# Optimization experiments

Hardware: AMD Instinct MI355X
Metric: run time of the kernel (lower is better)

## Reference

```python
import jax, jax.numpy as jnp
import numpy as np

B, SEQ_LEN, PRED_LEN, LABEL_LEN, PERIOD, N_CH = 32, 2048, 1024, 512, 256, 256
K = SEQ_LEN // PERIOD   # seg_num_x = 8
L = PRED_LEN // PERIOD  # seg_num_y = 4
EPS = 1e-5


def setup_inputs() -> dict:
    key = jax.random.key(0)
    k1, k2, k3, k4, k5, k6, k7 = jax.random.split(key, 7)
    x_enc = jax.random.normal(k1, (B, SEQ_LEN, N_CH), jnp.float32)
    x_mark_enc = jax.random.normal(k2, (B, SEQ_LEN, 4), jnp.float32)
    x_dec = jax.random.normal(k3, (B, LABEL_LEN + PRED_LEN, N_CH), jnp.float32)
    x_mark_dec = jax.random.normal(k4, (B, LABEL_LEN + PRED_LEN, 4), jnp.float32)
    # base_model abstracted as a linear map on the time axis of a [B, PERIOD, N] segment.
    # Scaled ~1/sqrt(P) so repeated powers (up to K+L-1 = 11) stay numerically tame.
    W_base = jax.random.normal(k5, (PERIOD, PERIOD), jnp.float32) * (0.9 / np.sqrt(PERIOD))
    # new_encoders[j]: nn.Linear(seg_num_x, 1) -> weight row [K] + bias scalar per j.
    W_enc = jax.random.normal(k6, (L, K), jnp.float32) * (1.0 / np.sqrt(K))
    b_enc = jax.random.normal(k7, (L,), jnp.float32) * 0.01
    return {"x_enc": x_enc, "x_mark_enc": x_mark_enc, "x_dec": x_dec,
            "x_mark_dec": x_mark_dec, "W_base": W_base, "W_enc": W_enc, "b_enc": b_enc}


def reference(x_enc, x_mark_enc, x_dec, x_mark_dec, W_base, W_enc, b_enc):
    Bv, S, N = x_enc.shape
    # per-series normalization over time (means is .detach()'d in torch; fwd math identical)
    means = jnp.mean(x_enc, axis=1, keepdims=True)                  # [B,1,N]
    xc = x_enc - means
    stdev = jnp.sqrt(jnp.var(xc, axis=1, keepdims=True) + EPS)      # [B,1,N]
    xn = xc / stdev

    # split into K segments of length PERIOD: [K, B, P, N]
    segs = xn.reshape(Bv, K, PERIOD, N).transpose(1, 0, 2, 3)

    # x_res[l][k] = base_model applied (K - k + l) times to segment k.
    # base(x) = einsum('qp,bpn->bqn', W_base, x), so m applications = W_base^m.
    def step(c, _):
        nxt = W_base @ c
        return nxt, nxt
    _, rest = jax.lax.scan(step, W_base, None, length=K + L - 2)
    powers = jnp.concatenate([W_base[None], rest], axis=0)          # powers[i] = W^(i+1)

    exps = (K - jnp.arange(K))[None, :] + jnp.arange(L)[:, None]    # [L,K]
    Wlk = powers[exps - 1]                                          # [L,K,P,P]
    x_res = jnp.einsum('lkqp,kbpn->lkbqn', Wlk, segs)               # [L,K,B,P,N]

    # dec_out_part[l] = sum_k W_enc[l,k] * x_res[l][k] + b_enc[l] * ones
    dec = jnp.einsum('lk,lkbqn->lbqn', W_enc, x_res) + b_enc[:, None, None, None]
    dec = dec.transpose(1, 0, 2, 3).reshape(Bv, L * PERIOD, N)      # cat over time

    # de-normalize
    dec = dec * stdev[:, 0, :][:, None, :] + means[:, 0, :][:, None, :]
    return dec[:, -PRED_LEN:, :]
```

## Files before the change

### kernel.cpp

```cpp
#include <hip/hip_runtime.h>
#include <cstdint>
#include <cstddef>


typedef unsigned short ushort_t;
typedef unsigned int uint_t;
typedef __attribute__((ext_vector_type(8))) short bf16x8;
typedef __attribute__((ext_vector_type(16))) float f32x16;

__device__ __forceinline__ ushort_t f32_to_bf16(float f) {
    uint_t u = __float_as_uint(f);
    u += 0x7FFFu + ((u >> 16) & 1u);
    return (ushort_t)(u >> 16);
}
__device__ __forceinline__ float bf16_to_f32(ushort_t h) {
    return __uint_as_float((uint_t)h << 16);
}

struct PowOps { int sa[4]; int sb[4]; int sd[4]; };

__global__ void powmul(const float* __restrict__ Wb, float* __restrict__ Pw, PowOps ops) {
    __shared__ float As[4 * 256];
    const int mat = blockIdx.x;
    const int r0  = blockIdx.y * 4;
    const int tid = threadIdx.x;
    const float* A  = (ops.sa[mat] < 0) ? Wb : Pw + (size_t)ops.sa[mat] * 65536;
    const float* Bm = (ops.sb[mat] < 0) ? Wb : Pw + (size_t)ops.sb[mat] * 65536;
    float* C        = Pw + (size_t)ops.sd[mat] * 65536;
#pragma unroll
    for (int i = 0; i < 4; ++i) As[i * 256 + tid] = A[(size_t)(r0 + i) * 256 + tid];
    __syncthreads();
    float a0 = 0.f, a1 = 0.f, a2 = 0.f, a3 = 0.f;
    for (int p = 0; p < 256; p += 8) {
        float bv[8];
#pragma unroll
        for (int u = 0; u < 8; ++u) bv[u] = Bm[(size_t)(p + u) * 256 + tid];
#pragma unroll
        for (int u = 0; u < 8; ++u) {
            a0 += As[0 * 256 + p + u] * bv[u];
            a1 += As[1 * 256 + p + u] * bv[u];
            a2 += As[2 * 256 + p + u] * bv[u];
            a3 += As[3 * 256 + p + u] * bv[u];
        }
    }
    C[(size_t)(r0 + 0) * 256 + tid] = a0;
    C[(size_t)(r0 + 1) * 256 + tid] = a1;
    C[(size_t)(r0 + 2) * 256 + tid] = a2;
    C[(size_t)(r0 + 3) * 256 + tid] = a3;
}

__global__ void prep(const float* __restrict__ x, ushort_t* __restrict__ Xt,
                     float* __restrict__ ps1, float* __restrict__ ps2,
                     const float* __restrict__ Pw, const float* __restrict__ Wb,
                     ushort_t* __restrict__ Pb, float* __restrict__ prs) {
    __shared__ float lds[64 * 65];
    __shared__ float red1[16 * 64];
    __shared__ float red2[16 * 64];
    const int bid = blockIdx.x;
    const int tid = threadIdx.x;
    if (bid < 4096) {
        const int st = bid & 31;
        const int nt = (bid >> 5) & 3;
        const int b  = bid >> 7;
        const int c = tid & 15, r = tid >> 4;
        const int s0 = st * 64;
        float s1[4] = {0,0,0,0}, s2[4] = {0,0,0,0};
#pragma unroll
        for (int it = 0; it < 4; ++it) {
            const int ii = r + it * 16;
            const float4 v = *(const float4*)(x + ((size_t)b * 2048 + s0 + ii) * 256 + nt * 64 + c * 4);
            const float vv[4] = {v.x, v.y, v.z, v.w};
#pragma unroll
            for (int jj = 0; jj < 4; ++jj) {
                lds[ii * 65 + c * 4 + jj] = vv[jj];
                s1[jj] += vv[jj]; s2[jj] += vv[jj] * vv[jj];
            }
        }
#pragma unroll
        for (int jj = 0; jj < 4; ++jj) { red1[r * 64 + c * 4 + jj] = s1[jj]; red2[r * 64 + c * 4 + jj] = s2[jj]; }
        __syncthreads();
        if (tid < 64) {
            float a = 0.f, q = 0.f;
#pragma unroll
            for (int rr = 0; rr < 16; ++rr) { a += red1[rr * 64 + tid]; q += red2[rr * 64 + tid]; }
            const size_t o = (size_t)st * 8192 + b * 256 + nt * 64 + tid;
            ps1[o] = a; ps2[o] = q;
        }
#pragma unroll
        for (int step = 0; step < 8; ++step) {
            const int npr = step * 8 + (tid >> 5);
            const int sp  = (tid & 31) * 2;
            const float f0 = lds[sp * 65 + npr];
            const float f1 = lds[(sp + 1) * 65 + npr];
            const uint_t packed = (uint_t)f32_to_bf16(f0) | ((uint_t)f32_to_bf16(f1) << 16);
            *(uint_t*)(Xt + ((size_t)b * 256 + nt * 64 + npr) * 2048 + s0 + sp) = packed;
        }
    } else {
        const int ib = bid - 4096;
        const int e  = ib >> 2;
        const int rq = ib & 3;
        const int q  = rq * 64 + (tid >> 2);
        const int cc = tid & 3;
        uint2* dst = (uint2*)(Pb + (size_t)e * 65536 + q * 256 + cc * 64);
        float s = 0.f;
        if (e == 0) {
#pragma unroll
            for (int i = 0; i < 16; ++i) {
                uint2 o; o.x = 0u; o.y = 0u;
                const int col0 = cc * 64 + i * 4;
                if (q >= col0 && q < col0 + 4) {
                    const int j = q - col0;
                    if (j == 0) o.x = 0x3F80u; else if (j == 1) o.x = 0x3F800000u;
                    else if (j == 2) o.y = 0x3F80u; else o.y = 0x3F800000u;
                }
                dst[i] = o;
            }
            s = 1.0f;
        } else {
            const float* src = (e == 1) ? Wb : (Pw + (size_t)(e - 2) * 65536);
            const float4* sp = (const float4*)(src + (size_t)q * 256 + cc * 64);
#pragma unroll
            for (int i = 0; i < 16; ++i) {
                const float4 v = sp[i];
                const ushort_t h0 = f32_to_bf16(v.x), h1 = f32_to_bf16(v.y);
                const ushort_t h2 = f32_to_bf16(v.z), h3 = f32_to_bf16(v.w);
                s += bf16_to_f32(h0) + bf16_to_f32(h1) + bf16_to_f32(h2) + bf16_to_f32(h3);
                uint2 o; o.x = (uint_t)h0 | ((uint_t)h1 << 16); o.y = (uint_t)h2 | ((uint_t)h3 << 16);
                dst[i] = o;
            }
        }
        s += __shfl_xor(s, 1);
        s += __shfl_xor(s, 2);
        if (cc == 0) prs[e * 256 + q] = s;
    }
}

#define GLOAD_LDS16(gsrc, ldst) \
    __builtin_amdgcn_global_load_lds((const __attribute__((address_space(1))) void*)(gsrc), \
                                     (__attribute__((address_space(3))) void*)(ldst), 16, 0, 0)

__global__ __launch_bounds__(256, 2) void gemm_v(
    const ushort_t* __restrict__ Pb,
    const ushort_t* __restrict__ Xt,
    ushort_t* __restrict__ vt,
    const float* __restrict__ ps1, const float* __restrict__ ps2,
    const float* __restrict__ prs, const float* __restrict__ Wenc,
    float* __restrict__ meanv, float* __restrict__ stdv, float* __restrict__ rsA)
{
    __shared__ ushort_t sAa[3][4096];
    __shared__ ushort_t sBb[3][8192];

    const int bid = blockIdx.x;
    const int tid = threadIdx.x;
    if (bid >= 512) {
        const int idx = bid - 512;
        if (idx < 32) {
            const int b = idx;
            float s = 0.f, q = 0.f;
#pragma unroll
            for (int st = 0; st < 32; ++st) {
                s += ps1[(size_t)st * 8192 + b * 256 + tid];
                q += ps2[(size_t)st * 8192 + b * 256 + tid];
            }
            const float mean = s * (1.0f / 2048.0f);
            float var = q * (1.0f / 2048.0f) - mean * mean;
            var = fmaxf(var, 0.0f);
            meanv[b * 256 + tid] = mean;
            stdv [b * 256 + tid] = sqrtf(var + 1e-5f);
        } else {
            const int l = idx - 32;
            float u = 0.f;
#pragma unroll
            for (int k = 0; k < 8; ++k) u += Wenc[l * 8 + k] * prs[(8 - k) * 256 + tid];
            float* uf = (float*)&sAa[0][0];
            uf[tid] = u;
            __syncthreads();
            const uint2* rp = (const uint2*)(Pb + (size_t)l * 65536 + tid * 256);
            float s = 0.f;
#pragma unroll
            for (int i = 0; i < 64; ++i) {
                const uint2 v = rp[i];
                s += bf16_to_f32((ushort_t)(v.x & 0xffff)) * uf[i * 4 + 0]
                   + bf16_to_f32((ushort_t)(v.x >> 16))    * uf[i * 4 + 1]
                   + bf16_to_f32((ushort_t)(v.y & 0xffff)) * uf[i * 4 + 2]
                   + bf16_to_f32((ushort_t)(v.y >> 16))    * uf[i * 4 + 3];
            }
            rsA[l * 256 + tid] = s;
        }
        return;
    }

    const int xcd  = bid & 7;
    const int g    = bid >> 3;
    const int colT = xcd + ((g & 7) << 3);
    const int k    = g >> 3;
    const int e    = 8 - k;

    const int lane = tid & 63;
    const int w    = tid >> 6;
    const int wm   = w >> 1, wn = w & 1;
    const int li   = lane & 31, lg = lane >> 5;
    const int lq3  = (li >> 1) & 3;
    const int lrow = 2 * (lane >> 3) + ((lane >> 2) & 1);
    const int kc   = (lane & 3) ^ ((lane >> 3) & 3);

    const ushort_t* xtb = Xt + (size_t)(colT * 128) * 2048 + k * 256;
    const ushort_t* pbb = Pb + (size_t)e * 65536;

#define VSTAGE(bf_, kt_) do { \
    const int p0_ = (kt_) * 32 + kc * 8; \
    GLOAD_LDS16(xtb + (size_t)(w * 32 + 0  + lrow) * 2048 + p0_, &sAa[bf_][(w * 32 + 0)  * 32]); \
    GLOAD_LDS16(xtb + (size_t)(w * 32 + 16 + lrow) * 2048 + p0_, &sAa[bf_][(w * 32 + 16) * 32]); \
    GLOAD_LDS16(pbb + (w * 64 + 0  + lrow) * 256 + p0_, &sBb[bf_][(w * 64 + 0)  * 32]); \
    GLOAD_LDS16(pbb + (w * 64 + 16 + lrow) * 256 + p0_, &sBb[bf_][(w * 64 + 16) * 32]); \
    GLOAD_LDS16(pbb + (w * 64 + 32 + lrow) * 256 + p0_, &sBb[bf_][(w * 64 + 32) * 32]); \
    GLOAD_LDS16(pbb + (w * 64 + 48 + lrow) * 256 + p0_, &sBb[bf_][(w * 64 + 48) * 32]); \
} while (0)

    f32x16 acc[2][4];
#pragma unroll
    for (int mm = 0; mm < 2; ++mm)
#pragma unroll
        for (int nn = 0; nn < 4; ++nn)
#pragma unroll
            for (int rr = 0; rr < 16; ++rr) acc[mm][nn][rr] = 0.0f;

    VSTAGE(0, 0);
    VSTAGE(1, 1);

#define VKT(kt_) do { \
    if ((kt_) < 7) { asm volatile("s_waitcnt vmcnt(6)" ::: "memory"); } \
    else           { asm volatile("s_waitcnt vmcnt(0)" ::: "memory"); } \
    __builtin_amdgcn_s_barrier(); \
    asm volatile("" ::: "memory"); \
    const ushort_t* pa_ = &sAa[(kt_) % 3][0]; \
    const ushort_t* px_ = &sBb[(kt_) % 3][0]; \
    bf16x8 af[2][2], xf[2][4]; \
    _Pragma("unroll") \
    for (int ks = 0; ks < 2; ++ks) { \
        const int sl = ((ks << 1) + lg) ^ lq3; \
        const int ro = (li >> 1) * 64 + (li & 1) * 32 + sl * 8; \
        af[ks][0] = *(const bf16x8*)(pa_ + wm * 2048 + ro); \
        af[ks][1] = *(const bf16x8*)(pa_ + wm * 2048 + 1024 + ro); \
        xf[ks][0] = *(const bf16x8*)(px_ + wn * 4096 + ro); \
        xf[ks][1] = *(const bf16x8*)(px_ + wn * 4096 + 1024 + ro); \
        xf[ks][2] = *(const bf16x8*)(px_ + wn * 4096 + 2048 + ro); \
        xf[ks][3] = *(const bf16x8*)(px_ + wn * 4096 + 3072 + ro); \
    } \
    if ((kt_) < 6) { VSTAGE(((kt_) + 2) % 3, (kt_) + 2); } \
    __builtin_amdgcn_s_setprio(1); \
    _Pragma("unroll") \
    for (int ks = 0; ks < 2; ++ks) \
        _Pragma("unroll") \
        for (int mm = 0; mm < 2; ++mm) \
            _Pragma("unroll") \
            for (int nn = 0; nn < 4; ++nn) \
                acc[mm][nn] = __builtin_amdgcn_mfma_f32_32x32x16_bf16(af[ks][mm], xf[ks][nn], acc[mm][nn], 0, 0, 0); \
    __builtin_amdgcn_s_setprio(0); \
    asm volatile("" ::: "memory"); \
} while (0)

    VKT(0); VKT(1); VKT(2); VKT(3); VKT(4); VKT(5); VKT(6); VKT(7);
#undef VKT
#undef VSTAGE

    ushort_t* vb = vt + (size_t)k * 2097152;
#pragma unroll
    for (int mm = 0; mm < 2; ++mm)
#pragma unroll
        for (int nn = 0; nn < 4; ++nn) {
            const int q = wn * 128 + nn * 32 + li;
#pragma unroll
            for (int rr = 0; rr < 16; ++rr) {
                const int c = colT * 128 + wm * 64 + mm * 32 + ((rr & 3) + 8 * (rr >> 2) + 4 * lg);
                vb[(size_t)c * 256 + q] = f32_to_bf16(acc[mm][nn][rr]);
            }
        }
}

__global__ void combine(const ushort_t* __restrict__ vt, const float* __restrict__ Wenc,
                        ushort_t* __restrict__ c) {
    const int t   = threadIdx.x;
    const int col = blockIdx.x * 8 + (t >> 5);
    const size_t off = (size_t)col * 256 + (t & 31) * 8;
    float a0[8] = {0,0,0,0,0,0,0,0}, a1[8] = {0,0,0,0,0,0,0,0};
    float a2[8] = {0,0,0,0,0,0,0,0}, a3[8] = {0,0,0,0,0,0,0,0};
#pragma unroll
    for (int k = 0; k < 8; ++k) {
        const bf16x8 v = *(const bf16x8*)(vt + (size_t)k * 2097152 + off);
        const float w0 = Wenc[0 * 8 + k], w1 = Wenc[1 * 8 + k];
        const float w2 = Wenc[2 * 8 + k], w3 = Wenc[3 * 8 + k];
#pragma unroll
        for (int j = 0; j < 8; ++j) {
            const float f = bf16_to_f32((ushort_t)v[j]);
            a0[j] += w0 * f; a1[j] += w1 * f; a2[j] += w2 * f; a3[j] += w3 * f;
        }
    }
    bf16x8 o0, o1, o2, o3;
#pragma unroll
    for (int j = 0; j < 8; ++j) {
        o0[j] = (short)f32_to_bf16(a0[j]); o1[j] = (short)f32_to_bf16(a1[j]);
        o2[j] = (short)f32_to_bf16(a2[j]); o3[j] = (short)f32_to_bf16(a3[j]);
    }
    *(bf16x8*)(c + 0 * 2097152 + off) = o0;
    *(bf16x8*)(c + 1 * 2097152 + off) = o1;
    *(bf16x8*)(c + 2 * 2097152 + off) = o2;
    *(bf16x8*)(c + 3 * 2097152 + off) = o3;
}

__global__ __launch_bounds__(256, 2) void gemm2(
    const ushort_t* __restrict__ Pb, const ushort_t* __restrict__ c,
    const float* __restrict__ meanv, const float* __restrict__ stdv,
    const float* __restrict__ rsA, const float* __restrict__ benc,
    float* __restrict__ out)
{
    __shared__ ushort_t sAa[3][4096];
    __shared__ ushort_t sBb[3][4096];

    const int bid  = blockIdx.x;
    const int xcd  = bid & 7;
    const int g    = bid >> 3;
    const int colT = xcd + ((g & 7) << 3);
    const int rest = g >> 3;
    const int l    = rest >> 1;
    const int qpT  = rest & 1;

    const int tid  = threadIdx.x;
    const int lane = tid & 63;
    const int w    = tid >> 6;
    const int wm   = w >> 1, wn = w & 1;
    const int li   = lane & 31, lg = lane >> 5;
    const int lq3  = (li >> 1) & 3;
    const int lrow = 2 * (lane >> 3) + ((lane >> 2) & 1);
    const int kc   = (lane & 3) ^ ((lane >> 3) & 3);

    const ushort_t* ab = Pb + (size_t)l * 65536 + (size_t)(qpT * 128) * 256;
    const ushort_t* cb = c + ((size_t)l * 8192 + colT * 128) * 256;

#define GSTAGE(bf_, kt_) do { \
    const int p0_ = (kt_) * 32 + kc * 8; \
// ... 56 lines not shown
        mn[nn] = meanv[col];
        sd[nn] = stdv [col];
    }
#pragma unroll
    for (int mm = 0; mm < 2; ++mm)
#pragma unroll
        for (int nn = 0; nn < 2; ++nn) {
            const int col = colT * 128 + wn * 64 + nn * 32 + li;
            const int bq = col >> 8, nq = col & 255;
            const float ben = be * sd[nn];
#pragma unroll
            for (int rr = 0; rr < 16; ++rr) {
                const int trow = l * 256 + qpT * 128 + wm * 64 + mm * 32
                               + ((rr & 3) + 8 * (rr >> 2) + 4 * lg);
                out[((size_t)bq * 1024 + trow) * 256 + nq] =
                    acc[mm][nn][rr] + mn[nn] * (1.0f - rsA[trow]) + ben;
            }
        }
}

extern "C" void kernel_launch(void* const* d_in, const int* in_sizes, int n_in,
                              void* d_out, int out_size, void* d_ws, size_t ws_size,
                              hipStream_t stream) {
    (void)in_sizes; (void)n_in; (void)out_size; (void)ws_size;
    const float* x_enc  = (const float*)d_in[0];
    const float* W_base = (const float*)d_in[4];
    const float* W_enc  = (const float*)d_in[5];
    const float* b_enc  = (const float*)d_in[6];
    float* out = (float*)d_out;

    char* ws = (char*)d_ws;
    float*    wsP    = (float*)(ws);
    ushort_t* wsPb   = (ushort_t*)(ws + 0x200000);
    float*    wsPrs  = (float*)(ws + 0x320000);
    float*    wsS1   = (float*)(ws + 0x330000);
    float*    wsS2   = (float*)(ws + 0x430000);
    float*    wsMean = (float*)(ws + 0x530000);
    float*    wsStd  = (float*)(ws + 0x540000);
    float*    wsRsA  = (float*)(ws + 0x550000);
    ushort_t* wsXt   = (ushort_t*)(ws + 0x600000);
    ushort_t* wsC    = (ushort_t*)(ws + 0x600000);
    ushort_t* wsVt   = (ushort_t*)(ws + 0x2600000);

    { PowOps o{{-1, 0, 0, 0}, {-1, 0, 0, 0}, {0, 0, 0, 0}};
      powmul<<<dim3(1, 64), 256, 0, stream>>>(W_base, wsP, o); }
    { PowOps o{{0, 0, 0, 0}, {-1, 0, 0, 0}, {1, 2, 0, 0}};
      powmul<<<dim3(2, 64), 256, 0, stream>>>(W_base, wsP, o); }
    { PowOps o{{2, 2, 2, 2}, {-1, 0, 1, 2}, {3, 4, 5, 6}};
      powmul<<<dim3(4, 64), 256, 0, stream>>>(W_base, wsP, o); }

    prep<<<4132, 256, 0, stream>>>(x_enc, wsXt, wsS1, wsS2, wsP, W_base, wsPb, wsPrs);

    gemm_v<<<548, 256, 0, stream>>>(wsPb, wsXt, wsVt, wsS1, wsS2, wsPrs, W_enc,
                                    wsMean, wsStd, wsRsA);

    combine<<<1024, 256, 0, stream>>>(wsVt, W_enc, wsC);

    gemm2<<<512, 256, 0, stream>>>(wsPb, wsC, wsMean, wsStd, wsRsA, b_enc, out);
}
```

Before: 98.77 us.

## Fuse input transpose, bf16 conversion and statistics into the first GEMM

The separate prep pass that transposed x_enc into a bf16 buffer and computed partial sums is removed. gemm_v now loads fp32 x tiles directly, accumulates sum and sum-of-squares in registers, and builds swizzled bf16 MFMA fragments in LDS through a scratch buffer. The mean/std and row-sum side work moves into the combine kernel. This drops a full write and read of the transposed activation tensor, but it adds LDS traffic, extra barriers and register pressure inside the GEMM main loop.

New measurement: 126.0 us. +27.6%, slower.

```diff
diff --git a/kernel.cpp b/kernel.cpp
--- a/kernel.cpp
+++ b/kernel.cpp
@@ -49,90 +49,45 @@
     C[(size_t)(r0 + 3) * 256 + tid] = a3;
 }
 
-__global__ void prep(const float* __restrict__ x, ushort_t* __restrict__ Xt,
-                     float* __restrict__ ps1, float* __restrict__ ps2,
-                     const float* __restrict__ Pw, const float* __restrict__ Wb,
-                     ushort_t* __restrict__ Pb, float* __restrict__ prs) {
-    __shared__ float lds[64 * 65];
-    __shared__ float red1[16 * 64];
-    __shared__ float red2[16 * 64];
-    const int bid = blockIdx.x;
+__global__ void prepPb(const float* __restrict__ Pw, const float* __restrict__ Wb,
+                       ushort_t* __restrict__ Pb, float* __restrict__ prs) {
+    const int ib = blockIdx.x;
+    const int e  = ib >> 2;
+    const int rq = ib & 3;
     const int tid = threadIdx.x;
-    if (bid < 4096) {
-        const int st = bid & 31;
-        const int nt = (bid >> 5) & 3;
-        const int b  = bid >> 7;
-        const int c = tid & 15, r = tid >> 4;
-        const int s0 = st * 64;
-        float s1[4] = {0,0,0,0}, s2[4] = {0,0,0,0};
-#pragma unroll
-        for (int it = 0; it < 4; ++it) {
-            const int ii = r + it * 16;
-            const float4 v = *(const float4*)(x + ((size_t)b * 2048 + s0 + ii) * 256 + nt * 64 + c * 4);
-            const float vv[4] = {v.x, v.y, v.z, v.w};
-#pragma unroll
-            for (int jj = 0; jj < 4; ++jj) {
-                lds[ii * 65 + c * 4 + jj] = vv[jj];
-                s1[jj] += vv[jj]; s2[jj] += vv[jj] * vv[jj];
+    const int q  = rq * 64 + (tid >> 2);
+    const int cc = tid & 3;
+    uint2* dst = (uint2*)(Pb + (size_t)e * 65536 + q * 256 + cc * 64);
+    float s = 0.f;
+    if (e == 0) {
+#pragma unroll
+        for (int i = 0; i < 16; ++i) {
+            uint2 o; o.x = 0u; o.y = 0u;
+            const int col0 = cc * 64 + i * 4;
+            if (q >= col0 && q < col0 + 4) {
+                const int j = q - col0;
+                if (j == 0) o.x = 0x3F80u; else if (j == 1) o.x = 0x3F800000u;
+                else if (j == 2) o.y = 0x3F80u; else o.y = 0x3F800000u;
             }
-        }
-#pragma unroll
-        for (int jj = 0; jj < 4; ++jj) { red1[r * 64 + c * 4 + jj] = s1[jj]; red2[r * 64 + c * 4 + jj] = s2[jj]; }
-        __syncthreads();
-        if (tid < 64) {
-            float a = 0.f, q = 0.f;
-#pragma unroll
-            for (int rr = 0; rr < 16; ++rr) { a += red1[rr * 64 + tid]; q += red2[rr * 64 + tid]; }
-            const size_t o = (size_t)st * 8192 + b * 256 + nt * 64 + tid;
-            ps1[o] = a; ps2[o] = q;
-        }
-#pragma unroll
-        for (int step = 0; step < 8; ++step) {
-            const int npr = step * 8 + (tid >> 5);
-            const int sp  = (tid & 31) * 2;
-            const float f0 = lds[sp * 65 + npr];
-            const float f1 = lds[(sp + 1) * 65 + npr];
-            const uint_t packed = (uint_t)f32_to_bf16(f0) | ((uint_t)f32_to_bf16(f1) << 16);
-            *(uint_t*)(Xt + ((size_t)b * 256 + nt * 64 + npr) * 2048 + s0 + sp) = packed;
-        }
+            dst[i] = o;
+        }
+        s = 1.0f;
     } else {
-        const int ib = bid - 4096;
-        const int e  = ib >> 2;
-        const int rq = ib & 3;
-        const int q  = rq * 64 + (tid >> 2);
-        const int cc = tid & 3;
-        uint2* dst = (uint2*)(Pb + (size_t)e * 65536 + q * 256 + cc * 64);
-        float s = 0.f;
-        if (e == 0) {
-#pragma unroll
-            for (int i = 0; i < 16; ++i) {
-                uint2 o; o.x = 0u; o.y = 0u;
-                const int col0 = cc * 64 + i * 4;
-                if (q >= col0 && q < col0 + 4) {
-                    const int j = q - col0;
-                    if (j == 0) o.x = 0x3F80u; else if (j == 1) o.x = 0x3F800000u;
-                    else if (j == 2) o.y = 0x3F80u; else o.y = 0x3F800000u;
-                }
-                dst[i] = o;
-            }
-            s = 1.0f;
-        } else {
-            const float* src = (e == 1) ? Wb : (Pw + (size_t)(e - 2) * 65536);
-            const float4* sp = (const float4*)(src + (size_t)q * 256 + cc * 64);
-#pragma unroll
-            for (int i = 0; i < 16; ++i) {
-                const float4 v = sp[i];
-                const ushort_t h0 = f32_to_bf16(v.x), h1 = f32_to_bf16(v.y);
-                const ushort_t h2 = f32_to_bf16(v.z), h3 = f32_to_bf16(v.w);
-                s += bf16_to_f32(h0) + bf16_to_f32(h1) + bf16_to_f32(h2) + bf16_to_f32(h3);
-                uint2 o; o.x = (uint_t)h0 | ((uint_t)h1 << 16); o.y = (uint_t)h2 | ((uint_t)h3 << 16);
-                dst[i] = o;
-            }
-        }
-        s += __shfl_xor(s, 1);
-        s += __shfl_xor(s, 2);
-        if (cc == 0) prs[e * 256 + q] = s;
-    }
+        const float* src = (e == 1) ? Wb : (Pw + (size_t)(e - 2) * 65536);
+        const float4* sp = (const float4*)(src + (size_t)q * 256 + cc * 64);
+#pragma unroll
+        for (int i = 0; i < 16; ++i) {
+            const float4 v = sp[i];
+            const ushort_t h0 = f32_to_bf16(v.x), h1 = f32_to_bf16(v.y);
+            const ushort_t h2 = f32_to_bf16(v.z), h3 = f32_to_bf16(v.w);
+            s += bf16_to_f32(h0) + bf16_to_f32(h1) + bf16_to_f32(h2) + bf16_to_f32(h3);
+            uint2 o; o.x = (uint_t)h0 | ((uint_t)h1 << 16); o.y = (uint_t)h2 | ((uint_t)h3 << 16);
+            dst[i] = o;
+        }
+    }
+    s += __shfl_xor(s, 1);
+    s += __shfl_xor(s, 2);
+    if (cc == 0) prs[e * 256 + q] = s;
 }
 
 #define GLOAD_LDS16(gsrc, ldst) \
@@ -140,62 +95,20 @@
                                      (__attribute__((address_space(3))) void*)(ldst), 16, 0, 0)
 
 __global__ __launch_bounds__(256, 2) void gemm_v(
-    const ushort_t* __restrict__ Pb,
-    const ushort_t* __restrict__ Xt,
+    const ushort_t* __restrict__ Pb, const float* __restrict__ x,
     ushort_t* __restrict__ vt,
-    const float* __restrict__ ps1, const float* __restrict__ ps2,
-    const float* __restrict__ prs, const float* __restrict__ Wenc,
-    float* __restrict__ meanv, float* __restrict__ stdv, float* __restrict__ rsA)
+    float* __restrict__ psS1, float* __restrict__ psS2)
 {
-    __shared__ ushort_t sAa[3][4096];
-    __shared__ ushort_t sBb[3][8192];
-
-    const int bid = blockIdx.x;
-    const int tid = threadIdx.x;
-    if (bid >= 512) {
-        const int idx = bid - 512;
-        if (idx < 32) {
-            const int b = idx;
-            float s = 0.f, q = 0.f;
-#pragma unroll
-            for (int st = 0; st < 32; ++st) {
-                s += ps1[(size_t)st * 8192 + b * 256 + tid];
-                q += ps2[(size_t)st * 8192 + b * 256 + tid];
-            }
-            const float mean = s * (1.0f / 2048.0f);
-            float var = q * (1.0f / 2048.0f) - mean * mean;
-            var = fmaxf(var, 0.0f);
-            meanv[b * 256 + tid] = mean;
-            stdv [b * 256 + tid] = sqrtf(var + 1e-5f);
-        } else {
-            const int l = idx - 32;
-            float u = 0.f;
-#pragma unroll
-            for (int k = 0; k < 8; ++k) u += Wenc[l * 8 + k] * prs[(8 - k) * 256 + tid];
-            float* uf = (float*)&sAa[0][0];
-            uf[tid] = u;
-            __syncthreads();
-            const uint2* rp = (const uint2*)(Pb + (size_t)l * 65536 + tid * 256);
-            float s = 0.f;
-#pragma unroll
-            for (int i = 0; i < 64; ++i) {
-                const uint2 v = rp[i];
-                s += bf16_to_f32((ushort_t)(v.x & 0xffff)) * uf[i * 4 + 0]
-                   + bf16_to_f32((ushort_t)(v.x >> 16))    * uf[i * 4 + 1]
-                   + bf16_to_f32((ushort_t)(v.y & 0xffff)) * uf[i * 4 + 2]
-                   + bf16_to_f32((ushort_t)(v.y >> 16))    * uf[i * 4 + 3];
-            }
-            rsA[l * 256 + tid] = s;
-        }
-        return;
-    }
-
-    const int xcd  = bid & 7;
-    const int g    = bid >> 3;
-    const int colT = xcd + ((g & 7) << 3);
-    const int k    = g >> 3;
+    __shared__ ushort_t sA[2][4096];
+    __shared__ ushort_t sB[3][8192];
+    __shared__ float    scr[32 * 128];
+
+    const int bid  = blockIdx.x;
+    const int k    = bid & 7;
+    const int colT = bid >> 3;
     const int e    = 8 - k;
 
+    const int tid  = threadIdx.x;
     const int lane = tid & 63;
     const int w    = tid >> 6;
     const int wm   = w >> 1, wn = w & 1;
@@ -204,17 +117,58 @@
     const int lrow = 2 * (lane >> 3) + ((lane >> 2) & 1);
     const int kc   = (lane & 3) ^ ((lane >> 3) & 3);
 
-    const ushort_t* xtb = Xt + (size_t)(colT * 128) * 2048 + k * 256;
     const ushort_t* pbb = Pb + (size_t)e * 65536;
-
-#define VSTAGE(bf_, kt_) do { \
+    const int b  = colT >> 1;
+    const int n0 = (colT & 1) * 128;
+    const float* xseg = x + ((size_t)b * 2048 + k * 256) * 256 + n0;
+
+    const int xp = tid >> 5;
+    const int xn = (tid & 31) * 4;
+
+    float4 xr[4];
+    float s1[4] = {0, 0, 0, 0}, s2[4] = {0, 0, 0, 0};
+
+#define BSTAGE(bf_, kt_) do { \
     const int p0_ = (kt_) * 32 + kc * 8; \
-    GLOAD_LDS16(xtb + (size_t)(w * 32 + 0  + lrow) * 2048 + p0_, &sAa[bf_][(w * 32 + 0)  * 32]); \
-    GLOAD_LDS16(xtb + (size_t)(w * 32 + 16 + lrow) * 2048 + p0_, &sAa[bf_][(w * 32 + 16) * 32]); \
-    GLOAD_LDS16(pbb + (w * 64 + 0  + lrow) * 256 + p0_, &sBb[bf_][(w * 64 + 0)  * 32]); \
-    GLOAD_LDS16(pbb + (w * 64 + 16 + lrow) * 256 + p0_, &sBb[bf_][(w * 64 + 16) * 32]); \
-    GLOAD_LDS16(pbb + (w * 64 + 32 + lrow) * 256 + p0_, &sBb[bf_][(w * 64 + 32) * 32]); \
-    GLOAD_LDS16(pbb + (w * 64 + 48 + lrow) * 256 + p0_, &sBb[bf_][(w * 64 + 48) * 32]); \
+    GLOAD_LDS16(pbb + (w * 64 + 0  + lrow) * 256 + p0_, &sB[bf_][(w * 64 + 0)  * 32]); \
+    GLOAD_LDS16(pbb + (w * 64 + 16 + lrow) * 256 + p0_, &sB[bf_][(w * 64 + 16) * 32]); \
+    GLOAD_LDS16(pbb + (w * 64 + 32 + lrow) * 256 + p0_, &sB[bf_][(w * 64 + 32) * 32]); \
+    GLOAD_LDS16(pbb + (w * 64 + 48 + lrow) * 256 + p0_, &sB[bf_][(w * 64 + 48) * 32]); \
+} while (0)
+
+#define XLOAD(kt_) do { \
+    _Pragma("unroll") \
+    for (int i_ = 0; i_ < 4; ++i_) \
+        xr[i_] = *(const float4*)(xseg + (size_t)((kt_) * 32 + xp + 8 * i_) * 256 + xn); \
+} while (0)
+
+#define SCRW() do { \
+    _Pragma("unroll") \
+    for (int i_ = 0; i_ < 4; ++i_) { \
+        *(float4*)(scr + (xp + 8 * i_) * 128 + xn) = xr[i_]; \
+        s1[0] += xr[i_].x; s2[0] += xr[i_].x * xr[i_].x; \
+        s1[1] += xr[i_].y; s2[1] += xr[i_].y * xr[i_].y; \
+        s1[2] += xr[i_].z; s2[2] += xr[i_].z * xr[i_].z; \
+        s1[3] += xr[i_].w; s2[3] += xr[i_].w * xr[i_].w; \
+    } \
+} while (0)
+
+#define FRAGBUILD(buf_) do { \
+    const int R_ = tid >> 1; \
+    const int swz_ = (R_ >> 1) & 3; \
+    _Pragma("unroll") \
+    for (int cc_ = 0; cc_ < 2; ++cc_) { \
+        const int pc_ = (tid & 1) * 2 + cc_; \
+        uint_t pk_[4]; \
+        _Pragma("unroll") \
+        for (int u_ = 0; u_ < 4; ++u_) { \
+            const float v0_ = scr[(pc_ * 8 + 2 * u_ + 0) * 128 + R_]; \
+            const float v1_ = scr[(pc_ * 8 + 2 * u_ + 1) * 128 + R_]; \
+            pk_[u_] = (uint_t)f32_to_bf16(v0_) | ((uint_t)f32_to_bf16(v1_) << 16); \
+        } \
+        uint4 o_; o_.x = pk_[0]; o_.y = pk_[1]; o_.z = pk_[2]; o_.w = pk_[3]; \
+        *(uint4*)((char*)&sA[buf_][0] + R_ * 64 + ((pc_ ^ swz_) << 4)) = o_; \
+    } \
 } while (0)
 
     f32x16 acc[2][4];
@@ -225,16 +179,26 @@
 #pragma unroll
             for (int rr = 0; rr < 16; ++rr) acc[mm][nn][rr] = 0.0f;
 
-    VSTAGE(0, 0);
-    VSTAGE(1, 1);
+    XLOAD(0);
+    SCRW();
+    asm volatile("s_waitcnt lgkmcnt(0)" ::: "memory");
+    __builtin_amdgcn_s_barrier();
+    asm volatile("" ::: "memory");
+    FRAGBUILD(0);
+    BSTAGE(0, 0);
+    asm volatile("" ::: "memory");
+    XLOAD(1);
+    asm volatile("" ::: "memory");
+    BSTAGE(1, 1);
+    asm volatile("s_waitcnt lgkmcnt(0)" ::: "memory");
 
 #define VKT(kt_) do { \
-    if ((kt_) < 7) { asm volatile("s_waitcnt vmcnt(6)" ::: "memory"); } \
+    if ((kt_) < 7) { asm volatile("s_waitcnt vmcnt(4)" ::: "memory"); } \
     else           { asm volatile("s_waitcnt vmcnt(0)" ::: "memory"); } \
     __builtin_amdgcn_s_barrier(); \
     asm volatile("" ::: "memory"); \
-    const ushort_t* pa_ = &sAa[(kt_) % 3][0]; \
-    const ushort_t* px_ = &sBb[(kt_) % 3][0]; \
+    const ushort_t* pa_ = &sA[(kt_) & 1][0]; \
+    const ushort_t* px_ = &sB[(kt_) % 3][0]; \
     bf16x8 af[2][2], xf[2][4]; \
     _Pragma("unroll") \
     for (int ks = 0; ks < 2; ++ks) { \
@@ -247,7 +211,12 @@
         xf[ks][2] = *(const bf16x8*)(px_ + wn * 4096 + 2048 + ro); \
         xf[ks][3] = *(const bf16x8*)(px_ + wn * 4096 + 3072 + ro); \
     } \
-    if ((kt_) < 6) { VSTAGE(((kt_) + 2) % 3, (kt_) + 2); } \
+    if ((kt_) < 7) { SCRW(); }    \
+    if ((kt_) < 6) { \
+        XLOAD((kt_) + 2); \
+        asm volatile("" ::: "memory"); \
+        BSTAGE(((kt_) + 2) % 3, (kt_) + 2); \
+    } \
     __builtin_amdgcn_s_setprio(1); \
     _Pragma("unroll") \
     for (int ks = 0; ks < 2; ++ks) \
@@ -258,11 +227,21 @@
                 acc[mm][nn] = __builtin_amdgcn_mfma_f32_32x32x16_bf16(af[ks][mm], xf[ks][nn], acc[mm][nn], 0, 0, 0); \
     __builtin_amdgcn_s_setprio(0); \
     asm volatile("" ::: "memory"); \
+    if ((kt_) < 7) { \
+        asm volatile("s_waitcnt lgkmcnt(0)" ::: "memory"); \
+        __builtin_amdgcn_s_barrier(); \
+        asm volatile("" ::: "memory"); \
+        FRAGBUILD(((kt_) + 1) & 1); \
+        asm volatile("s_waitcnt lgkmcnt(0)" ::: "memory"); \
+    } \
 } while (0)
 
     VKT(0); VKT(1); VKT(2); VKT(3); VKT(4); VKT(5); VKT(6); VKT(7);
 #undef VKT
-#undef VSTAGE
+#undef FRAGBUILD
+#undef SCRW
+#undef XLOAD
+#undef BSTAGE
 
     ushort_t* vb = vt + (size_t)k * 2097152;
 #pragma unroll
@@ -276,36 +255,96 @@
                 vb[(size_t)c * 256 + q] = f32_to_bf16(acc[mm][nn][rr]);
             }
         }
+
+    __syncthreads();
+#pragma unroll
+    for (int j = 0; j < 4; ++j) {
+        scr[xp * 128 + xn + j]        = s1[j];
+        scr[1024 + xp * 128 + xn + j] = s2[j];
+    }
+    __syncthreads();
+    if (tid < 128) {
+        float a = 0.f;
+#pragma unroll
+        for (int r = 0; r < 8; ++r) a += scr[r * 128 + tid];
+        psS1[(size_t)k * 8192 + colT * 128 + tid] = a;
+    } else {
+        const int tt = tid - 128;
+        float a = 0.f;
+#pragma unroll
+        for (int r = 0; r < 8; ++r) a += scr[1024 + r * 128 + tt];
+        psS2[(size_t)k * 8192 + colT * 128 + tt] = a;
+    }
 }
 
 __global__ void combine(const ushort_t* __restrict__ vt, const float* __restrict__ Wenc,
-                        ushort_t* __restrict__ c) {
+                        ushort_t* __restrict__ c,
+                        const float* __restrict__ psS1, const float* __restrict__ psS2,
+                        const float* __restrict__ prs, const ushort_t* __restrict__ Pb,
+                        float* __restrict__ meanv, float* __restrict__ stdv,
+                        float* __restrict__ rsA) {
+    __shared__ float uf[256];
+    const int bid = blockIdx.x;
     const int t   = threadIdx.x;
-    const int col = blockIdx.x * 8 + (t >> 5);
-    const size_t off = (size_t)col * 256 + (t & 31) * 8;
-    float a0[8] = {0,0,0,0,0,0,0,0}, a1[8] = {0,0,0,0,0,0,0,0};
-    float a2[8] = {0,0,0,0,0,0,0,0}, a3[8] = {0,0,0,0,0,0,0,0};
-#pragma unroll
-    for (int k = 0; k < 8; ++k) {
-        const bf16x8 v = *(const bf16x8*)(vt + (size_t)k * 2097152 + off);
-        const float w0 = Wenc[0 * 8 + k], w1 = Wenc[1 * 8 + k];
-        const float w2 = Wenc[2 * 8 + k], w3 = Wenc[3 * 8 + k];
+    if (bid < 1024) {
+        const int col = bid * 8 + (t >> 5);
+        const size_t off = (size_t)col * 256 + (t & 31) * 8;
+        float a0[8] = {0,0,0,0,0,0,0,0}, a1[8] = {0,0,0,0,0,0,0,0};
+        float a2[8] = {0,0,0,0,0,0,0,0}, a3[8] = {0,0,0,0,0,0,0,0};
+#pragma unroll
+        for (int k = 0; k < 8; ++k) {
+            const bf16x8 v = *(const bf16x8*)(vt + (size_t)k * 2097152 + off);
+            const float w0 = Wenc[0 * 8 + k], w1 = Wenc[1 * 8 + k];
+            const float w2 = Wenc[2 * 8 + k], w3 = Wenc[3 * 8 + k];
+#pragma unroll
+            for (int j = 0; j < 8; ++j) {
+                const float f = bf16_to_f32((ushort_t)v[j]);
+                a0[j] += w0 * f; a1[j] += w1 * f; a2[j] += w2 * f; a3[j] += w3 * f;
+            }
+        }
+        bf16x8 o0, o1, o2, o3;
 #pragma unroll
         for (int j = 0; j < 8; ++j) {
-            const float f = bf16_to_f32((ushort_t)v[j]);
-            a0[j] += w0 * f; a1[j] += w1 * f; a2[j] += w2 * f; a3[j] += w3 * f;
-        }
-    }
-    bf16x8 o0, o1, o2, o3;
-#pragma unroll
-    for (int j = 0; j < 8; ++j) {
-        o0[j] = (short)f32_to_bf16(a0[j]); o1[j] = (short)f32_to_bf16(a1[j]);
-        o2[j] = (short)f32_to_bf16(a2[j]); o3[j] = (short)f32_to_bf16(a3[j]);
-    }
-    *(bf16x8*)(c + 0 * 2097152 + off) = o0;
-    *(bf16x8*)(c + 1 * 2097152 + off) = o1;
-    *(bf16x8*)(c + 2 * 2097152 + off) = o2;
-    *(bf16x8*)(c + 3 * 2097152 + off) = o3;
+            o0[j] = (short)f32_to_bf16(a0[j]); o1[j] = (short)f32_to_bf16(a1[j]);
+            o2[j] = (short)f32_to_bf16(a2[j]); o3[j] = (short)f32_to_bf16(a3[j]);
+        }
+        *(bf16x8*)(c + 0 * 2097152 + off) = o0;
+        *(bf16x8*)(c + 1 * 2097152 + off) = o1;
+        *(bf16x8*)(c + 2 * 2097152 + off) = o2;
+        *(bf16x8*)(c + 3 * 2097152 + off) = o3;
+    } else if (bid < 1056) {
+        const int b = bid - 1024;
+        const int col = b * 256 + t;
+        float s = 0.f, q = 0.f;
+#pragma unroll
+        for (int k = 0; k < 8; ++k) {
+            s += psS1[(size_t)k * 8192 + col];
+            q += psS2[(size_t)k * 8192 + col];
+        }
+        const float mean = s * (1.0f / 2048.0f);
+        float var = q * (1.0f / 2048.0f) - mean * mean;
+        var = fmaxf(var, 0.0f);
+        meanv[col] = mean;
+        stdv [col] = sqrtf(var + 1e-5f);
+    } else {
+        const int l = bid - 1056;
+        float u = 0.f;
+#pragma unroll
+        for (int k = 0; k < 8; ++k) u += Wenc[l * 8 + k] * prs[(8 - k) * 256 + t];
+        uf[t] = u;
+        __syncthreads();
+        const uint2* rp = (const uint2*)(Pb + (size_t)l * 65536 + t * 256);
+        float s = 0.f;
+#pragma unroll
+        for (int i = 0; i < 64; ++i) {
+            const uint2 v = rp[i];
+            s += bf16_to_f32((ushort_t)(v.x & 0xffff)) * uf[i * 4 + 0]
+               + bf16_to_f32((ushort_t)(v.x >> 16))    * uf[i * 4 + 1]
+               + bf16_to_f32((ushort_t)(v.y & 0xffff)) * uf[i * 4 + 2]
+               + bf16_to_f32((ushort_t)(v.y >> 16))    * uf[i * 4 + 3];
+        }
+        rsA[l * 256 + t] = s;
+    }
 }
 
 __global__ __launch_bounds__(256, 2) void gemm2(
@@ -428,15 +467,14 @@
     char* ws = (char*)d_ws;
     float*    wsP    = (float*)(ws);
     ushort_t* wsPb   = (ushort_t*)(ws + 0x200000);
-    float*    wsPrs  = (float*)(ws + 0x320000);
-    float*    wsS1   = (float*)(ws + 0x330000);
-    float*    wsS2   = (float*)(ws + 0x430000);
-    float*    wsMean = (float*)(ws + 0x530000);
-    float*    wsStd  = (float*)(ws + 0x540000);
-    float*    wsRsA  = (float*)(ws + 0x550000);
-    ushort_t* wsXt   = (ushort_t*)(ws + 0x600000);
-    ushort_t* wsC    = (ushort_t*)(ws + 0x600000);
-    ushort_t* wsVt   = (ushort_t*)(ws + 0x2600000);
+    float*    wsPrs  = (float*)(ws + 0x340000);
+    float*    wsS1   = (float*)(ws + 0x350000);
+    float*    wsS2   = (float*)(ws + 0x390000);
+    float*    wsMean = (float*)(ws + 0x3D0000);
+    float*    wsStd  = (float*)(ws + 0x3E0000);
+    float*    wsRsA  = (float*)(ws + 0x3F0000);
+    ushort_t* wsVt   = (ushort_t*)(ws + 0x400000);
+    ushort_t* wsC    = (ushort_t*)(ws + 0x2400000);
 
     { PowOps o{{-1, 0, 0, 0}, {-1, 0, 0, 0}, {0, 0, 0, 0}};
       powmul<<<dim3(1, 64), 256, 0, stream>>>(W_base, wsP, o); }
@@ -445,12 +483,12 @@
     { PowOps o{{2, 2, 2, 2}, {-1, 0, 1, 2}, {3, 4, 5, 6}};
       powmul<<<dim3(4, 64), 256, 0, stream>>>(W_base, wsP, o); }
 
-    prep<<<4132, 256, 0, stream>>>(x_enc, wsXt, wsS1, wsS2, wsP, W_base, wsPb, wsPrs);
-
-    gemm_v<<<548, 256, 0, stream>>>(wsPb, wsXt, wsVt, wsS1, wsS2, wsPrs, W_enc,
-                                    wsMean, wsStd, wsRsA);
-
-    combine<<<1024, 256, 0, stream>>>(wsVt, W_enc, wsC);
+    prepPb<<<36, 256, 0, stream>>>(wsP, W_base, wsPb, wsPrs);
+
+    gemm_v<<<512, 256, 0, stream>>>(wsPb, x_enc, wsVt, wsS1, wsS2);
+
+    combine<<<1060, 256, 0, stream>>>(wsVt, W_enc, wsC, wsS1, wsS2, wsPrs, wsPb,
+                                      wsMean, wsStd, wsRsA);
 
     gemm2<<<512, 256, 0, stream>>>(wsPb, wsC, wsMean, wsStd, wsRsA, b_enc, out);
 }
```

## Fuse bf16 power conversion into powmul and move stats blocks to combine

Applied to the files above, without the earlier changes.

The power-matrix kernel now writes the bf16 copy of each power (identity, W, and higher powers) and its row sums directly. This removes the 36 conversion blocks from prep. The mean/std and rsA side blocks move out of the gemm_v launch into the combine launch, so the main GEMM grid has no tail blocks. The risk is a longer critical path in the small powmul launches, plus some extra work in combine.

Result: no change. 99.64 us (+0.9%).

```diff
diff --git a/kernel.cpp b/kernel.cpp
--- a/kernel.cpp
+++ b/kernel.cpp
@@ -17,121 +17,112 @@
     return __uint_as_float((uint_t)h << 16);
 }
 
-struct PowOps { int sa[4]; int sb[4]; int sd[4]; };
-
-__global__ void powmul(const float* __restrict__ Wb, float* __restrict__ Pw, PowOps ops) {
+struct PowOps { int sa[4]; int sb[4]; int sd[4]; int ed[4]; };
+
+__global__ void powmulc(const float* __restrict__ Wb, float* __restrict__ Pw,
+                        ushort_t* __restrict__ Pb, float* __restrict__ prs, PowOps ops) {
     __shared__ float As[4 * 256];
+    __shared__ float red[4][4];
     const int mat = blockIdx.x;
     const int r0  = blockIdx.y * 4;
     const int tid = threadIdx.x;
-    const float* A  = (ops.sa[mat] < 0) ? Wb : Pw + (size_t)ops.sa[mat] * 65536;
-    const float* Bm = (ops.sb[mat] < 0) ? Wb : Pw + (size_t)ops.sb[mat] * 65536;
-    float* C        = Pw + (size_t)ops.sd[mat] * 65536;
-#pragma unroll
-    for (int i = 0; i < 4; ++i) As[i * 256 + tid] = A[(size_t)(r0 + i) * 256 + tid];
+    const int e   = ops.ed[mat];
+    const int sa  = ops.sa[mat];
+    float a[4];
+    if (sa == -2) {
+#pragma unroll
+        for (int i = 0; i < 4; ++i) a[i] = (r0 + i == tid) ? 1.0f : 0.0f;
+    } else if (sa == -3) {
+#pragma unroll
+        for (int i = 0; i < 4; ++i) a[i] = Wb[(size_t)(r0 + i) * 256 + tid];
+    } else {
+        const float* A  = (sa < 0) ? Wb : Pw + (size_t)sa * 65536;
+        const float* Bm = (ops.sb[mat] < 0) ? Wb : Pw + (size_t)ops.sb[mat] * 65536;
+#pragma unroll
+        for (int i = 0; i < 4; ++i) As[i * 256 + tid] = A[(size_t)(r0 + i) * 256 + tid];
+        __syncthreads();
+        float a0 = 0.f, a1 = 0.f, a2 = 0.f, a3 = 0.f;
+        for (int p = 0; p < 256; p += 8) {
+            float bv[8];
+#pragma unroll
+            for (int u = 0; u < 8; ++u) bv[u] = Bm[(size_t)(p + u) * 256 + tid];
+#pragma unroll
+            for (int u = 0; u < 8; ++u) {
+                a0 += As[0 * 256 + p + u] * bv[u];
+                a1 += As[1 * 256 + p + u] * bv[u];
+                a2 += As[2 * 256 + p + u] * bv[u];
+                a3 += As[3 * 256 + p + u] * bv[u];
+            }
+        }
+        a[0] = a0; a[1] = a1; a[2] = a2; a[3] = a3;
+        if (ops.sd[mat] >= 0) {
+            float* C = Pw + (size_t)ops.sd[mat] * 65536;
+#pragma unroll
+            for (int i = 0; i < 4; ++i) C[(size_t)(r0 + i) * 256 + tid] = a[i];
+        }
+        __syncthreads();
+    }
+    const int lane = tid & 63, wv = tid >> 6;
+    float rs[4];
+#pragma unroll
+    for (int i = 0; i < 4; ++i) {
+        const ushort_t h = f32_to_bf16(a[i]);
+        Pb[(size_t)e * 65536 + (size_t)(r0 + i) * 256 + tid] = h;
+        float v = bf16_to_f32(h);
+        v += __shfl_xor(v, 1);  v += __shfl_xor(v, 2);  v += __shfl_xor(v, 4);
+        v += __shfl_xor(v, 8);  v += __shfl_xor(v, 16); v += __shfl_xor(v, 32);
+        rs[i] = v;
+    }
+    if (lane == 0) {
+#pragma unroll
+        for (int i = 0; i < 4; ++i) red[i][wv] = rs[i];
+    }
     __syncthreads();
-    float a0 = 0.f, a1 = 0.f, a2 = 0.f, a3 = 0.f;
-    for (int p = 0; p < 256; p += 8) {
-        float bv[8];
-#pragma unroll
-        for (int u = 0; u < 8; ++u) bv[u] = Bm[(size_t)(p + u) * 256 + tid];
-#pragma unroll
-        for (int u = 0; u < 8; ++u) {
-            a0 += As[0 * 256 + p + u] * bv[u];
-            a1 += As[1 * 256 + p + u] * bv[u];
-            a2 += As[2 * 256 + p + u] * bv[u];
-            a3 += As[3 * 256 + p + u] * bv[u];
-        }
-    }
-    C[(size_t)(r0 + 0) * 256 + tid] = a0;
-    C[(size_t)(r0 + 1) * 256 + tid] = a1;
-    C[(size_t)(r0 + 2) * 256 + tid] = a2;
-    C[(size_t)(r0 + 3) * 256 + tid] = a3;
+    if (tid < 4) prs[e * 256 + r0 + tid] = red[tid][0] + red[tid][1] + red[tid][2] + red[tid][3];
 }
 
 __global__ void prep(const float* __restrict__ x, ushort_t* __restrict__ Xt,
-                     float* __restrict__ ps1, float* __restrict__ ps2,
-                     const float* __restrict__ Pw, const float* __restrict__ Wb,
-                     ushort_t* __restrict__ Pb, float* __restrict__ prs) {
+                     float* __restrict__ ps1, float* __restrict__ ps2) {
     __shared__ float lds[64 * 65];
     __shared__ float red1[16 * 64];
     __shared__ float red2[16 * 64];
     const int bid = blockIdx.x;
+    const int st = bid & 31;
+    const int nt = (bid >> 5) & 3;
+    const int b  = bid >> 7;
     const int tid = threadIdx.x;
-    if (bid < 4096) {
-        const int st = bid & 31;
-        const int nt = (bid >> 5) & 3;
-        const int b  = bid >> 7;
-        const int c = tid & 15, r = tid >> 4;
-        const int s0 = st * 64;
-        float s1[4] = {0,0,0,0}, s2[4] = {0,0,0,0};
-#pragma unroll
-        for (int it = 0; it < 4; ++it) {
-            const int ii = r + it * 16;
-            const float4 v = *(const float4*)(x + ((size_t)b * 2048 + s0 + ii) * 256 + nt * 64 + c * 4);
-            const float vv[4] = {v.x, v.y, v.z, v.w};
-#pragma unroll
-            for (int jj = 0; jj < 4; ++jj) {
-                lds[ii * 65 + c * 4 + jj] = vv[jj];
-                s1[jj] += vv[jj]; s2[jj] += vv[jj] * vv[jj];
-            }
-        }
-#pragma unroll
-        for (int jj = 0; jj < 4; ++jj) { red1[r * 64 + c * 4 + jj] = s1[jj]; red2[r * 64 + c * 4 + jj] = s2[jj]; }
-        __syncthreads();
-        if (tid < 64) {
-            float a = 0.f, q = 0.f;
-#pragma unroll
-            for (int rr = 0; rr < 16; ++rr) { a += red1[rr * 64 + tid]; q += red2[rr * 64 + tid]; }
-            const size_t o = (size_t)st * 8192 + b * 256 + nt * 64 + tid;
-            ps1[o] = a; ps2[o] = q;
-        }
-#pragma unroll
-        for (int step = 0; step < 8; ++step) {
-            const int npr = step * 8 + (tid >> 5);
-            const int sp  = (tid & 31) * 2;
-            const float f0 = lds[sp * 65 + npr];
-            const float f1 = lds[(sp + 1) * 65 + npr];
-            const uint_t packed = (uint_t)f32_to_bf16(f0) | ((uint_t)f32_to_bf16(f1) << 16);
-            *(uint_t*)(Xt + ((size_t)b * 256 + nt * 64 + npr) * 2048 + s0 + sp) = packed;
-        }
-    } else {
-        const int ib = bid - 4096;
-        const int e  = ib >> 2;
-        const int rq = ib & 3;
-        const int q  = rq * 64 + (tid >> 2);
-        const int cc = tid & 3;
-        uint2* dst = (uint2*)(Pb + (size_t)e * 65536 + q * 256 + cc * 64);
-        float s = 0.f;
-        if (e == 0) {
-#pragma unroll
-            for (int i = 0; i < 16; ++i) {
-                uint2 o; o.x = 0u; o.y = 0u;
-                const int col0 = cc * 64 + i * 4;
-                if (q >= col0 && q < col0 + 4) {
-                    const int j = q - col0;
-                    if (j == 0) o.x = 0x3F80u; else if (j == 1) o.x = 0x3F800000u;
-                    else if (j == 2) o.y = 0x3F80u; else o.y = 0x3F800000u;
-                }
-                dst[i] = o;
-            }
-            s = 1.0f;
-        } else {
-            const float* src = (e == 1) ? Wb : (Pw + (size_t)(e - 2) * 65536);
-            const float4* sp = (const float4*)(src + (size_t)q * 256 + cc * 64);
-#pragma unroll
-            for (int i = 0; i < 16; ++i) {
-                const float4 v = sp[i];
-                const ushort_t h0 = f32_to_bf16(v.x), h1 = f32_to_bf16(v.y);
-                const ushort_t h2 = f32_to_bf16(v.z), h3 = f32_to_bf16(v.w);
-                s += bf16_to_f32(h0) + bf16_to_f32(h1) + bf16_to_f32(h2) + bf16_to_f32(h3);
-                uint2 o; o.x = (uint_t)h0 | ((uint_t)h1 << 16); o.y = (uint_t)h2 | ((uint_t)h3 << 16);
-                dst[i] = o;
-            }
-        }
-        s += __shfl_xor(s, 1);
-        s += __shfl_xor(s, 2);
-        if (cc == 0) prs[e * 256 + q] = s;
+    const int c = tid & 15, r = tid >> 4;
+    const int s0 = st * 64;
+    float s1[4] = {0,0,0,0}, s2[4] = {0,0,0,0};
+#pragma unroll
+    for (int it = 0; it < 4; ++it) {
+        const int ii = r + it * 16;
+        const float4 v = *(const float4*)(x + ((size_t)b * 2048 + s0 + ii) * 256 + nt * 64 + c * 4);
+        const float vv[4] = {v.x, v.y, v.z, v.w};
+#pragma unroll
+        for (int jj = 0; jj < 4; ++jj) {
+            lds[ii * 65 + c * 4 + jj] = vv[jj];
+            s1[jj] += vv[jj]; s2[jj] += vv[jj] * vv[jj];
+        }
+    }
+#pragma unroll
+    for (int jj = 0; jj < 4; ++jj) { red1[r * 64 + c * 4 + jj] = s1[jj]; red2[r * 64 + c * 4 + jj] = s2[jj]; }
+    __syncthreads();
+    if (tid < 64) {
+        float a = 0.f, q = 0.f;
+#pragma unroll
+        for (int rr = 0; rr < 16; ++rr) { a += red1[rr * 64 + tid]; q += red2[rr * 64 + tid]; }
+        const size_t o = (size_t)st * 8192 + b * 256 + nt * 64 + tid;
+        ps1[o] = a; ps2[o] = q;
+    }
+#pragma unroll
+    for (int step = 0; step < 8; ++step) {
+        const int npr = step * 8 + (tid >> 5);
+        const int sp  = (tid & 31) * 2;
+        const float f0 = lds[sp * 65 + npr];
+        const float f1 = lds[(sp + 1) * 65 + npr];
+        const uint_t packed = (uint_t)f32_to_bf16(f0) | ((uint_t)f32_to_bf16(f1) << 16);
+        *(uint_t*)(Xt + ((size_t)b * 256 + nt * 64 + npr) * 2048 + s0 + sp) = packed;
     }
 }
 
@@ -142,53 +133,13 @@
 __global__ __launch_bounds__(256, 2) void gemm_v(
     const ushort_t* __restrict__ Pb,
     const ushort_t* __restrict__ Xt,
-    ushort_t* __restrict__ vt,
-    const float* __restrict__ ps1, const float* __restrict__ ps2,
-    const float* __restrict__ prs, const float* __restrict__ Wenc,
-    float* __restrict__ meanv, float* __restrict__ stdv, float* __restrict__ rsA)
+    ushort_t* __restrict__ vt)
 {
     __shared__ ushort_t sAa[3][4096];
     __shared__ ushort_t sBb[3][8192];
 
     const int bid = blockIdx.x;
     const int tid = threadIdx.x;
-    if (bid >= 512) {
-        const int idx = bid - 512;
-        if (idx < 32) {
-            const int b = idx;
-            float s = 0.f, q = 0.f;
-#pragma unroll
-            for (int st = 0; st < 32; ++st) {
-                s += ps1[(size_t)st * 8192 + b * 256 + tid];
-                q += ps2[(size_t)st * 8192 + b * 256 + tid];
-            }
-            const float mean = s * (1.0f / 2048.0f);
-            float var = q * (1.0f / 2048.0f) - mean * mean;
-            var = fmaxf(var, 0.0f);
-            meanv[b * 256 + tid] = mean;
-            stdv [b * 256 + tid] = sqrtf(var + 1e-5f);
-        } else {
-            const int l = idx - 32;
-            float u = 0.f;
-#pragma unroll
-            for (int k = 0; k < 8; ++k) u += Wenc[l * 8 + k] * prs[(8 - k) * 256 + tid];
-            float* uf = (float*)&sAa[0][0];
-            uf[tid] = u;
-            __syncthreads();
-            const uint2* rp = (const uint2*)(Pb + (size_t)l * 65536 + tid * 256);
-            float s = 0.f;
-#pragma unroll
-            for (int i = 0; i < 64; ++i) {
-                const uint2 v = rp[i];
-                s += bf16_to_f32((ushort_t)(v.x & 0xffff)) * uf[i * 4 + 0]
-                   + bf16_to_f32((ushort_t)(v.x >> 16))    * uf[i * 4 + 1]
-                   + bf16_to_f32((ushort_t)(v.y & 0xffff)) * uf[i * 4 + 2]
-                   + bf16_to_f32((ushort_t)(v.y >> 16))    * uf[i * 4 + 3];
-            }
-            rsA[l * 256 + tid] = s;
-        }
-        return;
-    }
 
     const int xcd  = bid & 7;
     const int g    = bid >> 3;
@@ -279,33 +230,72 @@
 }
 
 __global__ void combine(const ushort_t* __restrict__ vt, const float* __restrict__ Wenc,
-                        ushort_t* __restrict__ c) {
+                        ushort_t* __restrict__ c,
+                        const float* __restrict__ ps1, const float* __restrict__ ps2,
+                        const float* __restrict__ prs, const ushort_t* __restrict__ Pb,
+                        float* __restrict__ meanv, float* __restrict__ stdv,
+                        float* __restrict__ rsA) {
+    __shared__ float uf[256];
+    const int bid = blockIdx.x;
     const int t   = threadIdx.x;
-    const int col = blockIdx.x * 8 + (t >> 5);
-    const size_t off = (size_t)col * 256 + (t & 31) * 8;
-    float a0[8] = {0,0,0,0,0,0,0,0}, a1[8] = {0,0,0,0,0,0,0,0};
-    float a2[8] = {0,0,0,0,0,0,0,0}, a3[8] = {0,0,0,0,0,0,0,0};
-#pragma unroll
-    for (int k = 0; k < 8; ++k) {
-        const bf16x8 v = *(const bf16x8*)(vt + (size_t)k * 2097152 + off);
-        const float w0 = Wenc[0 * 8 + k], w1 = Wenc[1 * 8 + k];
-        const float w2 = Wenc[2 * 8 + k], w3 = Wenc[3 * 8 + k];
+    if (bid < 1024) {
+        const int col = bid * 8 + (t >> 5);
+        const size_t off = (size_t)col * 256 + (t & 31) * 8;
+        float a0[8] = {0,0,0,0,0,0,0,0}, a1[8] = {0,0,0,0,0,0,0,0};
+        float a2[8] = {0,0,0,0,0,0,0,0}, a3[8] = {0,0,0,0,0,0,0,0};
+#pragma unroll
+        for (int k = 0; k < 8; ++k) {
+            const bf16x8 v = *(const bf16x8*)(vt + (size_t)k * 2097152 + off);
+            const float w0 = Wenc[0 * 8 + k], w1 = Wenc[1 * 8 + k];
+            const float w2 = Wenc[2 * 8 + k], w3 = Wenc[3 * 8 + k];
+#pragma unroll
+            for (int j = 0; j < 8; ++j) {
+                const float f = bf16_to_f32((ushort_t)v[j]);
+                a0[j] += w0 * f; a1[j] += w1 * f; a2[j] += w2 * f; a3[j] += w3 * f;
+            }
+        }
+        bf16x8 o0, o1, o2, o3;
 #pragma unroll
         for (int j = 0; j < 8; ++j) {
-            const float f = bf16_to_f32((ushort_t)v[j]);
-            a0[j] += w0 * f; a1[j] += w1 * f; a2[j] += w2 * f; a3[j] += w3 * f;
-        }
-    }
-    bf16x8 o0, o1, o2, o3;
-#pragma unroll
-    for (int j = 0; j < 8; ++j) {
-        o0[j] = (short)f32_to_bf16(a0[j]); o1[j] = (short)f32_to_bf16(a1[j]);
-        o2[j] = (short)f32_to_bf16(a2[j]); o3[j] = (short)f32_to_bf16(a3[j]);
-    }
-    *(bf16x8*)(c + 0 * 2097152 + off) = o0;
-    *(bf16x8*)(c + 1 * 2097152 + off) = o1;
-    *(bf16x8*)(c + 2 * 2097152 + off) = o2;
-    *(bf16x8*)(c + 3 * 2097152 + off) = o3;
+            o0[j] = (short)f32_to_bf16(a0[j]); o1[j] = (short)f32_to_bf16(a1[j]);
+            o2[j] = (short)f32_to_bf16(a2[j]); o3[j] = (short)f32_to_bf16(a3[j]);
+        }
+        *(bf16x8*)(c + 0 * 2097152 + off) = o0;
+        *(bf16x8*)(c + 1 * 2097152 + off) = o1;
+        *(bf16x8*)(c + 2 * 2097152 + off) = o2;
+        *(bf16x8*)(c + 3 * 2097152 + off) = o3;
+    } else if (bid < 1056) {
+        const int b = bid - 1024;
+        float s = 0.f, q = 0.f;
+#pragma unroll
+        for (int st = 0; st < 32; ++st) {
+            s += ps1[(size_t)st * 8192 + b * 256 + t];
+            q += ps2[(size_t)st * 8192 + b * 256 + t];
+        }
+        const float mean = s * (1.0f / 2048.0f);
+        float var = q * (1.0f / 2048.0f) - mean * mean;
+        var = fmaxf(var, 0.0f);
+        meanv[b * 256 + t] = mean;
+        stdv [b * 256 + t] = sqrtf(var + 1e-5f);
+    } else {
+        const int l = bid - 1056;
+        float u = 0.f;
+#pragma unroll
+        for (int k = 0; k < 8; ++k) u += Wenc[l * 8 + k] * prs[(8 - k) * 256 + t];
+        uf[t] = u;
+        __syncthreads();
+        const uint2* rp = (const uint2*)(Pb + (size_t)l * 65536 + t * 256);
+        float s = 0.f;
+#pragma unroll
+        for (int i = 0; i < 64; ++i) {
+            const uint2 v = rp[i];
+            s += bf16_to_f32((ushort_t)(v.x & 0xffff)) * uf[i * 4 + 0]
+               + bf16_to_f32((ushort_t)(v.x >> 16))    * uf[i * 4 + 1]
+               + bf16_to_f32((ushort_t)(v.y & 0xffff)) * uf[i * 4 + 2]
+               + bf16_to_f32((ushort_t)(v.y >> 16))    * uf[i * 4 + 3];
+        }
+        rsA[l * 256 + t] = s;
+    }
 }
 
 __global__ __launch_bounds__(256, 2) void gemm2(
@@ -428,29 +418,29 @@
     char* ws = (char*)d_ws;
     float*    wsP    = (float*)(ws);
     ushort_t* wsPb   = (ushort_t*)(ws + 0x200000);
-    float*    wsPrs  = (float*)(ws + 0x320000);
-    float*    wsS1   = (float*)(ws + 0x330000);
-    float*    wsS2   = (float*)(ws + 0x430000);
-    float*    wsMean = (float*)(ws + 0x530000);
-    float*    wsStd  = (float*)(ws + 0x540000);
-    float*    wsRsA  = (float*)(ws + 0x550000);
+    float*    wsPrs  = (float*)(ws + 0x340000);
+    float*    wsS1   = (float*)(ws + 0x350000);
+    float*    wsS2   = (float*)(ws + 0x450000);
+    float*    wsMean = (float*)(ws + 0x550000);
+    float*    wsStd  = (float*)(ws + 0x560000);
+    float*    wsRsA  = (float*)(ws + 0x570000);
     ushort_t* wsXt   = (ushort_t*)(ws + 0x600000);
     ushort_t* wsC    = (ushort_t*)(ws + 0x600000);
     ushort_t* wsVt   = (ushort_t*)(ws + 0x2600000);
 
-    { PowOps o{{-1, 0, 0, 0}, {-1, 0, 0, 0}, {0, 0, 0, 0}};
-      powmul<<<dim3(1, 64), 256, 0, stream>>>(W_base, wsP, o); }
-    { PowOps o{{0, 0, 0, 0}, {-1, 0, 0, 0}, {1, 2, 0, 0}};
-      powmul<<<dim3(2, 64), 256, 0, stream>>>(W_base, wsP, o); }
-    { PowOps o{{2, 2, 2, 2}, {-1, 0, 1, 2}, {3, 4, 5, 6}};
-      powmul<<<dim3(4, 64), 256, 0, stream>>>(W_base, wsP, o); }
-
-    prep<<<4132, 256, 0, stream>>>(x_enc, wsXt, wsS1, wsS2, wsP, W_base, wsPb, wsPrs);
-
-    gemm_v<<<548, 256, 0, stream>>>(wsPb, wsXt, wsVt, wsS1, wsS2, wsPrs, W_enc,
-                                    wsMean, wsStd, wsRsA);
-
-    combine<<<1024, 256, 0, stream>>>(wsVt, W_enc, wsC);
+    { PowOps o{{-1, -3, -2, 0}, {-1, 0, 0, 0}, {0, -1, -1, 0}, {2, 1, 0, 0}};
+      powmulc<<<dim3(3, 64), 256, 0, stream>>>(W_base, wsP, wsPb, wsPrs, o); }
+    { PowOps o{{0, 0, 0, 0}, {-1, 0, 0, 0}, {1, 2, 0, 0}, {3, 4, 0, 0}};
+      powmulc<<<dim3(2, 64), 256, 0, stream>>>(W_base, wsP, wsPb, wsPrs, o); }
+    { PowOps o{{2, 2, 2, 2}, {-1, 0, 1, 2}, {-1, -1, -1, -1}, {5, 6, 7, 8}};
+      powmulc<<<dim3(4, 64), 256, 0, stream>>>(W_base, wsP, wsPb, wsPrs, o); }
+
+    prep<<<4096, 256, 0, stream>>>(x_enc, wsXt, wsS1, wsS2);
+
+    gemm_v<<<512, 256, 0, stream>>>(wsPb, wsXt, wsVt);
+
+    combine<<<1060, 256, 0, stream>>>(wsVt, W_enc, wsC, wsS1, wsS2, wsPrs, wsPb,
+                                      wsMean, wsStd, wsRsA);
 
     gemm2<<<512, 256, 0, stream>>>(wsPb, wsC, wsMean, wsStd, wsRsA, b_enc, out);
 }
```
